# Kernel optimization log

Measured on AMD Instinct MI355X. Metric: run time of the kernel, lower is better.

The kernel has to match this reference:

```python
import jax, jax.numpy as jnp
import numpy as np

SCORE_THR = 0.5
RADII = jnp.array([0.5, 0.6, 0.7], dtype=jnp.float32)  # radius_dict[c]; all labels 0..C-1 covered

B, N, C = 2, 8192, 3


def setup_inputs() -> dict:
    key = jax.random.key(0)
    k1, k2 = jax.random.split(key)
    xyz = jax.random.normal(k1, (B, N, 3), dtype=jnp.float32)
    cls_features = jax.random.normal(k2, (B, N, C), dtype=jnp.float32)
    return {"xyz": xyz, "cls_features": cls_features}


def _greedy_select(xyz, cls_features):
    """Greedy per-class radius suppression over the flattened batch.
    Returns sample_idx (B, L) int32, zero-padded exactly like the torch code
    (sample_idx is zeros except slot i of the batch owning selection i)."""
    b, n, _ = xyz.shape
    L = b * n
    scores = jax.nn.sigmoid(jnp.max(cls_features, axis=2))   # (B, N)
    labels = jnp.argmax(cls_features, axis=2)                # (B, N)
    valid = scores >= SCORE_THR

    flat_scores = jnp.where(valid, scores, -jnp.inf).reshape(L)
    order = jnp.argsort(-flat_scores)                        # descending score; invalid sink to end
    sorted_labels = labels.reshape(L)[order]
    sorted_valid = valid.reshape(L)[order]
    sorted_batch = (order // n).astype(jnp.int32)
    sorted_pts = xyz.reshape(L, 3)[order]

    def cond(state):
        i, remaining, _ = state
        return remaining.any() & (i < L)

    def body(state):
        i, remaining, sel_pos = state
        cur = jnp.argmax(remaining)                  # first remaining point in sorted order
        # NB: faithful to the original bug: radius chosen via sorted_labels[i]
        # (loop counter), not the label of the current point.
        r = RADII[sorted_labels[i]]
        d2 = jnp.sum((sorted_pts - sorted_pts[cur]) ** 2, axis=-1)  # (L,)
        suppress = (sorted_batch == sorted_batch[cur]) & (d2 <= r * r)
        return (i + 1, remaining & ~suppress, sel_pos.at[i].set(cur.astype(jnp.int32)))

    sel0 = jnp.full((L,), -1, dtype=jnp.int32)
    _, _, sel_pos = jax.lax.while_loop(cond, body, (jnp.int32(0), sorted_valid, sel0))

    picked = sel_pos >= 0
    orig = jnp.where(picked, order[jnp.maximum(sel_pos, 0)], 0)  # flat index in [0, L)
    bidx = jnp.where(picked, orig // n, 0)
    pidx = jnp.where(picked, orig % n, 0)
    slots = jnp.arange(L)
    # zeros init + scatter exactly mirrors torch: sample_idx[batch, i] = point
    sample_idx = jnp.zeros((b, L), dtype=jnp.int32).at[bidx, slots].set(pidx.astype(jnp.int32))
    return sample_idx


def reference(xyz, cls_features):
    sample_idx = _greedy_select(xyz, cls_features)
    bsz = xyz.shape[0]
    # gather_operation: new_xyz[b, m] = xyz[b, sample_idx[b, m]]
    new_xyz = xyz[jnp.arange(bsz)[:, None], sample_idx]          # (B, L, 3)
    return new_xyz, sample_idx
```

## Files before the change

kernel.cpp:

```cpp
#include <hip/hip_runtime.h>
#include <stdint.h>


#define L_TOT 16384
#define NPT   8192

__device__ __forceinline__ int cellco(float v) {
    int c = (int)floorf((v + 6.4f) * 1.25f);
    return c < 0 ? 0 : (c > 15 ? 15 : c);
}
__device__ __forceinline__ float d2f(float ax, float ay, float az,
                                     float bx, float by, float bz) {
    float dx = __fsub_rn(ax, bx), dy = __fsub_rn(ay, by), dz = __fsub_rn(az, bz);
    return __fadd_rn(__fadd_rn(__fmul_rn(dx, dx), __fmul_rn(dy, dy)), __fmul_rn(dz, dz));
}
__device__ __forceinline__ float rad2(int lb) {
    float rr = (lb == 0) ? 0.5f : ((lb == 1) ? 0.6f : 0.7f);
    return __fmul_rn(rr, rr);
}
__device__ __forceinline__ float rlf(float v, int l) {
    return __uint_as_float(__builtin_amdgcn_readlane(__float_as_uint(v), l));
}
__device__ __forceinline__ int rli(int v, int l) {
    return (int)__builtin_amdgcn_readlane((uint32_t)v, l);
}

__global__ void k1_keys(const float* __restrict__ cls, uint64_t* __restrict__ keys,
                        uint8_t* __restrict__ umeta, uint16_t* __restrict__ sample,
                        int* __restrict__ cellcnt, uint32_t* __restrict__ slab2) {
    int l = blockIdx.x * blockDim.x + threadIdx.x;
    if (l >= L_TOT) return;
    ((uint32_t*)sample)[l] = 0;
    if (l < 8192) cellcnt[l] = 0;
    if (l < 1024) slab2[l] = 0;
    float c0 = cls[l * 3 + 0], c1 = cls[l * 3 + 1], c2 = cls[l * 3 + 2];
    float m = c0; int lab = 0;
    if (c1 > m) { m = c1; lab = 1; }
    if (c2 > m) { m = c2; lab = 2; }
    int valid = (m >= 0.0f) ? 1 : 0;
    float keyf = valid ? m : -__builtin_inff();
    uint32_t u = __float_as_uint(keyf);
    uint32_t o = (u & 0x80000000u) ? ~u : (u | 0x80000000u);
    keys[l] = ((uint64_t)(~o) << 32) | (uint32_t)l;
    umeta[l] = (uint8_t)(lab | (valid << 2));
}

__global__ void __launch_bounds__(256) k2_sort(
    const uint64_t* __restrict__ keys, const uint8_t* __restrict__ umeta,
    const float* __restrict__ xyz,
    float4* __restrict__ spts, uint32_t* __restrict__ slab2, uint16_t* __restrict__ sorder,
    int* __restrict__ cellcnt) {
    __shared__ uint64_t tile[2048];
    __shared__ int psum[256];
    const int t = threadIdx.x;
    const int elem = t & 31, part = t >> 5;
    const int l = blockIdx.x * 32 + elem;
    const uint64_t myk = keys[l];
    int cnt = 0;
    for (int t0 = 0; t0 < L_TOT; t0 += 2048) {
        for (int j = t; j < 2048; j += 256) tile[j] = keys[t0 + j];
        __syncthreads();
        const int b0 = part * 256;
        #pragma unroll 4
        for (int j = 0; j < 256; ++j) cnt += (tile[b0 + j] < myk) ? 1 : 0;
        __syncthreads();
    }
    psum[t] = cnt;
    __syncthreads();
    if (t < 32) {
        int rank = 0;
        #pragma unroll
        for (int q = 0; q < 8; ++q) rank += psum[q * 32 + t];
        const int ll = blockIdx.x * 32 + t;
        int b = ll >> 13, p = ll & (NPT - 1);
        const float* src = xyz + ((size_t)(b * NPT + p)) * 3;
        float x = src[0], y = src[1], z = src[2];
        uint8_t mt = umeta[ll];
        int lab = mt & 3, valid = (mt >> 2) & 1;
        float4 v; v.x = x; v.y = y; v.z = z;
        v.w = __uint_as_float((uint32_t)(b | (valid << 1)));
        spts[rank] = v;
        sorder[rank] = (uint16_t)ll;
        atomicOr(&slab2[rank >> 4], (uint32_t)lab << ((rank & 15) << 1));
        if (valid) {
            int cl = (b << 12) | (cellco(z) << 8) | (cellco(y) << 4) | cellco(x);
            atomicAdd(&cellcnt[cl], 1);
        }
    }
}

__global__ void g2_scan(int* __restrict__ cellcnt, int* __restrict__ cellstart) {
    __shared__ int part[256];
    __shared__ int poff[256];
    int t = threadIdx.x;
    int base = t * 32;
    int loc[32];
    int s = 0;
    for (int k = 0; k < 32; ++k) { loc[k] = cellcnt[base + k]; s += loc[k]; }
    part[t] = s;
    __syncthreads();
    if (t == 0) {
        int run = 0;
        for (int q = 0; q < 256; ++q) { poff[q] = run; run += part[q]; }
    }
    __syncthreads();
    int run = poff[t];
    for (int k = 0; k < 32; ++k) {
        cellstart[base + k] = run; run += loc[k];
        cellcnt[base + k] = 0;
    }
    if (t == 255) cellstart[8192] = run;
}

__global__ void g3_scatter(const float4* __restrict__ spts, const int* __restrict__ cellstart,
                           int* __restrict__ cellfill, float4* __restrict__ cellxyz) {
    int pos = blockIdx.x * blockDim.x + threadIdx.x;
    if (pos >= L_TOT) return;
    float4 v = spts[pos];
    uint32_t w = __float_as_uint(v.w);
    if (!(w & 2u)) return;
    int b = (int)(w & 1u);
    int cl = (b << 12) | (cellco(v.z) << 8) | (cellco(v.y) << 4) | cellco(v.x);
    int slot = atomicAdd(&cellfill[cl], 1);
    float4 o; o.x = v.x; o.y = v.y; o.z = v.z; o.w = __uint_as_float((uint32_t)pos);
    cellxyz[cellstart[cl] + slot] = o;
}

__global__ void __launch_bounds__(1024) k3_greedy(
    const float4* __restrict__ spts, const uint32_t* __restrict__ slab2,
    const uint16_t* __restrict__ sorder,
    const int* __restrict__ cellstart, const float4* __restrict__ cellxyz,
    uint16_t* __restrict__ sample) {
    __shared__ uint64_t qpack[16384];
    __shared__ uint32_t rem[512];
    __shared__ uint32_t alive2[512];
    __shared__ uint16_t cs16[8194];
    __shared__ uint32_t slds2[1024];
    __shared__ float4   pkd[2][128];
    __shared__ int      pkb[2][128];
    __shared__ int      pkn[2];

    const int t = threadIdx.x;
    const int V = cellstart[8192];
    const int NPH = (V + 127) >> 7;

    float4 cv0 = make_float4(0,0,0,0), cv1 = make_float4(0,0,0,0);
    int cord0 = 0, cord1 = 0;
    if (t < 64) {
        cv0 = spts[t]; cv1 = spts[64 + t];
        cord0 = (int)sorder[t]; cord1 = (int)sorder[64 + t];
    }
    for (int j = t; j < 8193; j += 1024) cs16[j] = (uint16_t)cellstart[j];
    for (int j = t; j < 1024; j += 1024) slds2[j] = slab2[j];
    for (int k = t; k < V; k += 1024) {
        float4 q = cellxyz[k];
        int qx = __float2int_rn(__fmul_rn(__fadd_rn(q.x, 8.0f), 4096.0f));
        int qy = __float2int_rn(__fmul_rn(__fadd_rn(q.y, 8.0f), 4096.0f));
        int qz = __float2int_rn(__fmul_rn(__fadd_rn(q.z, 8.0f), 4096.0f));
        qx = qx < 0 ? 0 : (qx > 65535 ? 65535 : qx);
        qy = qy < 0 ? 0 : (qy > 65535 ? 65535 : qy);
        qz = qz < 0 ? 0 : (qz > 65535 ? 65535 : qz);
        uint32_t pos = __float_as_uint(q.w);
        qpack[k] = ((uint64_t)(((uint32_t)qz) | (pos << 16)) << 32)
                 | ((uint32_t)qx | ((uint32_t)qy << 16));
    }
    for (int w = t; w < 512; w += 1024) {
        int lo = w * 32;
        uint32_t m;
        if (V >= lo + 32) m = 0xFFFFFFFFu;
        else if (V <= lo) m = 0u;
        else m = (1u << (V - lo)) - 1u;
        rem[w] = m;
        alive2[w] = m;
    }
    if (t < 2) pkn[t] = 0;
    __syncthreads();

    int ii = 0;
    for (int ph = 0; ph < NPH; ++ph) {
        const int cur = ph & 1, prv = cur ^ 1;
        if (t < 64) {
            const int nb = (ph + 1) << 7;
            int q0 = nb + t;       q0 = q0 > (L_TOT - 1) ? (L_TOT - 1) : q0;
            int q1 = nb + 64 + t;  q1 = q1 > (L_TOT - 1) ? (L_TOT - 1) : q1;
            float4 nv0 = spts[q0], nv1 = spts[q1];
            int nord0 = (int)sorder[q0], nord1 = (int)sorder[q1];

            int o0 = ii + t;      o0 = o0 > (L_TOT - 1) ? (L_TOT - 1) : o0;
            int o1 = ii + 64 + t; o1 = o1 > (L_TOT - 1) ? (L_TOT - 1) : o1;
            float cr0 = rad2((int)((slds2[o0 >> 4] >> ((o0 & 15) << 1)) & 3u));
            float cr1 = rad2((int)((slds2[o1 >> 4] >> ((o1 & 15) << 1)) & 3u));

            const int pos0 = (ph << 7) + t, pos1 = pos0 + 64;
            bool a0 = (pos0 < V) && ((rem[pos0 >> 5] >> (pos0 & 31)) & 1u);
            bool a1 = (pos1 < V) && ((rem[pos1 >> 5] >> (pos1 & 31)) & 1u);
            const int cb0 = cord0 >> 13, cb1 = cord1 >> 13;
            if (__ballot((a0 ? 1 : 0) | (a1 ? 1 : 0))) {
                const int m = pkn[prv];
                for (int j = 0; j < m; ++j) {
                    float4 pk = pkd[prv][j];
                    int pb = pkb[prv][j];
                    if (a0 && cb0 == pb &&
                        d2f(cv0.x, cv0.y, cv0.z, pk.x, pk.y, pk.z) <= pk.w) a0 = false;
                    if (a1 && cb1 == pb &&
                        d2f(cv1.x, cv1.y, cv1.z, pk.x, pk.y, pk.z) <= pk.w) a1 = false;
                }
            }

            int np = 0;
            const int ii0 = ii;
            {
                unsigned long long am = __ballot(a0 ? 1 : 0);
                while (am) {
                    const int jl0 = (int)__builtin_ctzll(am);
                    const unsigned long long am2 = am & (am - 1);
                    const bool has2 = (am2 != 0ull);
                    const int jl1 = has2 ? (int)__builtin_ctzll(am2) : jl0;
                    const float p0x = rlf(cv0.x, jl0), p0y = rlf(cv0.y, jl0), p0z = rlf(cv0.z, jl0);
                    const int   b0  = rli(cord0, jl0) >> 13;
                    const float p1x = rlf(cv0.x, jl1), p1y = rlf(cv0.y, jl1), p1z = rlf(cv0.z, jl1);
                    const int   b1  = rli(cord0, jl1) >> 13;
                    const float r2_0 = rlf((np & 64) ? cr1 : cr0, np & 63);
                    const int np1 = np + 1;
                    const float r2_1 = rlf((np1 & 64) ? cr1 : cr0, np1 & 63);
                    const bool kb = (b0 == b1) &&
                                    (d2f(p1x, p1y, p1z, p0x, p0y, p0z) <= r2_0);
                    const bool two = has2 && !kb;
                    if (t == jl0) {
                        pkd[cur][np] = make_float4(cv0.x, cv0.y, cv0.z, r2_0);
                        pkb[cur][np] = b0;
                        sample[b0 * L_TOT + ii0 + np] = (uint16_t)(cord0 & (NPT - 1));
                    }
                    if (two && t == jl1) {
                        pkd[cur][np1] = make_float4(cv0.x, cv0.y, cv0.z, r2_1);
                        pkb[cur][np1] = b1;
                        sample[b1 * L_TOT + ii0 + np1] = (uint16_t)(cord0 & (NPT - 1));
                    }
                    if (a0) {
                        if (cb0 == b0 && d2f(cv0.x, cv0.y, cv0.z, p0x, p0y, p0z) <= r2_0) a0 = false;
                        if (two && cb0 == b1 && d2f(cv0.x, cv0.y, cv0.z, p1x, p1y, p1z) <= r2_1) a0 = false;
                    }
                    if (a1) {
                        if (cb1 == b0 && d2f(cv1.x, cv1.y, cv1.z, p0x, p0y, p0z) <= r2_0) a1 = false;
                        if (two && cb1 == b1 && d2f(cv1.x, cv1.y, cv1.z, p1x, p1y, p1z) <= r2_1) a1 = false;
                    }
                    np += two ? 2 : 1;
                    am = __ballot(a0 ? 1 : 0);
                }
            }
            {
                unsigned long long am = __ballot(a1 ? 1 : 0);
                while (am) {
                    const int jl0 = (int)__builtin_ctzll(am);
                    const unsigned long long am2 = am & (am - 1);
                    const bool has2 = (am2 != 0ull);
                    const int jl1 = has2 ? (int)__builtin_ctzll(am2) : jl0;
                    const float p0x = rlf(cv1.x, jl0), p0y = rlf(cv1.y, jl0), p0z = rlf(cv1.z, jl0);
                    const int   b0  = rli(cord1, jl0) >> 13;
                    const float p1x = rlf(cv1.x, jl1), p1y = rlf(cv1.y, jl1), p1z = rlf(cv1.z, jl1);
                    const int   b1  = rli(cord1, jl1) >> 13;
                    const float r2_0 = rlf((np & 64) ? cr1 : cr0, np & 63);
                    const int np1 = np + 1;
                    const float r2_1 = rlf((np1 & 64) ? cr1 : cr0, np1 & 63);
                    const bool kb = (b0 == b1) &&
                                    (d2f(p1x, p1y, p1z, p0x, p0y, p0z) <= r2_0);
                    const bool two = has2 && !kb;
                    if (t == jl0) {
                        pkd[cur][np] = make_float4(cv1.x, cv1.y, cv1.z, r2_0);
                        pkb[cur][np] = b0;
                        sample[b0 * L_TOT + ii0 + np] = (uint16_t)(cord1 & (NPT - 1));
                    }
                    if (two && t == jl1) {
                        pkd[cur][np1] = make_float4(cv1.x, cv1.y, cv1.z, r2_1);
                        pkb[cur][np1] = b1;
                        sample[b1 * L_TOT + ii0 + np1] = (uint16_t)(cord1 & (NPT - 1));
                    }
                    if (a1) {
                        if (cb1 == b0 && d2f(cv1.x, cv1.y, cv1.z, p0x, p0y, p0z) <= r2_0) a1 = false;
                        if (two && cb1 == b1 && d2f(cv1.x, cv1.y, cv1.z, p1x, p1y, p1z) <= r2_1) a1 = false;
                    }
                    np += two ? 2 : 1;
                    am = __ballot(a1 ? 1 : 0);
                }
            }
            ii = ii0 + np;
            if (t == 0) pkn[cur] = np;
            cv0 = nv0; cv1 = nv1; cord0 = nord0; cord1 = nord1;
        } else {
            const int np = pkn[prv];
            if (np > 0) {
                const int tid = t - 64;
                const int ntask = np * 216;
                for (int task = tid; task < ntask; task += 960) {
                    int sub = task & 7;
                    int pc = task >> 3;
                    int p = pc / 27;
                    int c = pc - p * 27;
                    float4 pv = pkd[prv][p];
                    int pb_ = pkb[prv][p];
                    float r2 = pv.w;
                    int cx = cellco(pv.x) + (c % 3) - 1;
                    int cy = cellco(pv.y) + ((c / 3) % 3) - 1;
                    int cz = cellco(pv.z) + (c / 9) - 1;
                    if ((unsigned)cx > 15u || (unsigned)cy > 15u || (unsigned)cz > 15u) continue;
                    float lox = -6.4f + 0.8f * cx, hix = lox + 0.8f;
                    float loy = -6.4f + 0.8f * cy, hiy = loy + 0.8f;
                    float loz = -6.4f + 0.8f * cz, hiz = loz + 0.8f;
                    if (cx == 0) lox = -1e30f;  if (cx == 15) hix = 1e30f;
                    if (cy == 0) loy = -1e30f;  if (cy == 15) hiy = 1e30f;
                    if (cz == 0) loz = -1e30f;  if (cz == 15) hiz = 1e30f;
                    float bdx = fmaxf(fmaxf(lox - pv.x, pv.x - hix), 0.0f);
                    float bdy = fmaxf(fmaxf(loy - pv.y, pv.y - hiy), 0.0f);
                    float bdz = fmaxf(fmaxf(loz - pv.z, pv.z - hiz), 0.0f);
                    if (bdx * bdx + bdy * bdy + bdz * bdz > r2 + 0.02f) continue;
                    int cl = (pb_ << 12) | (cz << 8) | (cy << 4) | cx;
                    int st = (int)cs16[cl];
                    int en = (int)cs16[cl + 1];
                    float psx = (pv.x + 8.0f) * 4096.0f;
                    float psy = (pv.y + 8.0f) * 4096.0f;
                    float psz = (pv.z + 8.0f) * 4096.0f;
                    float thr_hi = (r2 + 0.02f) * 16777216.0f;
                    float thr_lo = (r2 - 0.02f) * 16777216.0f;
                    for (int k = st + sub; k < en; k += 8) {
                        uint64_t e = qpack[k];
                        uint32_t lo = (uint32_t)e, hi = (uint32_t)(e >> 32);
                        float ddx = (float)(lo & 0xffffu) - psx;
                        float ddy = (float)(lo >> 16) - psy;
                        float ddz = (float)(hi & 0xffffu) - psz;
                        float d2s = ddx * ddx + ddy * ddy + ddz * ddz;
                        if (d2s <= thr_hi) {
                            if (alive2[k >> 5] & (1u << (k & 31))) {
                                bool sup = (d2s <= thr_lo);
                                if (!sup) {
                                    float4 q = cellxyz[k];
                                    sup = d2f(q.x, q.y, q.z, pv.x, pv.y, pv.z) <= r2;
                                }
                                if (sup) {
                                    uint32_t pos = hi >> 16;
                                    atomicAnd(&alive2[k >> 5], ~(1u << (k & 31)));
                                    atomicAnd(&rem[pos >> 5], ~(1u << (pos & 31)));
                                }
                            }
                        }
                    }
                }
            }
        }
        __syncthreads();
    }
}

__global__ void k4_out(const float* __restrict__ xyz, const uint16_t* __restrict__ sample,
                       float* __restrict__ out) {
    int s = blockIdx.x * blockDim.x + threadIdx.x;
    if (s >= 2 * L_TOT) return;
    int idx = (int)sample[s];
    int b = s >> 14;
    const float* src = xyz + ((size_t)(b * NPT + idx)) * 3;
    float* dst = out + (size_t)s * 3;
    dst[0] = src[0]; dst[1] = src[1]; dst[2] = src[2];
    out[3 * 2 * L_TOT + s] = (float)idx;
}

extern "C" void kernel_launch(void* const* d_in, const int* in_sizes, int n_in,
                              void* d_out, int out_size, void* d_ws, size_t ws_size,
                              hipStream_t stream) {
    const float* xyz = (const float*)d_in[0];
    const float* cls = (const float*)d_in[1];
    float* out = (float*)d_out;
    char* ws = (char*)d_ws;
    float4*   spts    = (float4*)  (ws + 0);
    uint32_t* slab2   = (uint32_t*)(ws + 262144);
    uint16_t* sorder  = (uint16_t*)(ws + 278528);
    int*      cellcnt = (int*)     (ws + 311296);
    int*      cellst  = (int*)     (ws + 344064);
    float4*   cellxyz = (float4*)  (ws + 380928);
    uint64_t* keys    = (uint64_t*)(ws + 380928);
    uint8_t*  umeta   = (uint8_t*) (ws + 512000);
    uint16_t* sample  = (uint16_t*)(ws + 643072);

    k1_keys   <<<64,  256, 0, stream>>>(cls, keys, umeta, sample, cellcnt, slab2);
    k2_sort   <<<512, 256, 0, stream>>>(keys, umeta, xyz, spts, slab2, sorder, cellcnt);
    g2_scan   <<<1,   256, 0, stream>>>(cellcnt, cellst);
    g3_scatter<<<64,  256, 0, stream>>>(spts, cellst, cellcnt, cellxyz);
    k3_greedy <<<1,  1024, 0, stream>>>(spts, slab2, sorder, cellst, cellxyz, sample);
    k4_out    <<<128, 256, 0, stream>>>(xyz, sample, out);
}
```

Before: 508.7 us.

## Replace phase-barrier greedy loop with asynchronous producer/consumer task queue

The greedy kernel drops the per-phase __syncthreads lockstep between the picking wavefront and the suppression workers. Wave 0 now publishes picks through an atomic counter, and workers claim per-pick, per-neighbour-cell tasks dynamically. Completion is tracked per pick so the picker only rechecks candidates against picks whose suppression has not finished. Pending picks are held in registers, and the alive2 filter and packed 2-bit label array are replaced by a byte label array. The intent is to overlap picking with suppression and remove barrier stalls, at the cost of spin-waiting, workgroup-scope atomics, and more redundant scanning, since each task now walks a whole cell serially.

After: 784.3 us. +54.2%, slower.

```diff
diff --git a/kernel.cpp b/kernel.cpp
--- a/kernel.cpp
+++ b/kernel.cpp
@@ -4,6 +4,7 @@
 
 #define L_TOT 16384
 #define NPT   8192
+#define WGS   __HIP_MEMORY_SCOPE_WORKGROUP
 
 __device__ __forceinline__ int cellco(float v) {
     int c = (int)floorf((v + 6.4f) * 1.25f);
@@ -27,12 +28,11 @@
 
 __global__ void k1_keys(const float* __restrict__ cls, uint64_t* __restrict__ keys,
                         uint8_t* __restrict__ umeta, uint16_t* __restrict__ sample,
-                        int* __restrict__ cellcnt, uint32_t* __restrict__ slab2) {
+                        int* __restrict__ cellcnt) {
     int l = blockIdx.x * blockDim.x + threadIdx.x;
     if (l >= L_TOT) return;
     ((uint32_t*)sample)[l] = 0;
     if (l < 8192) cellcnt[l] = 0;
-    if (l < 1024) slab2[l] = 0;
     float c0 = cls[l * 3 + 0], c1 = cls[l * 3 + 1], c2 = cls[l * 3 + 2];
     float m = c0; int lab = 0;
     if (c1 > m) { m = c1; lab = 1; }
@@ -48,7 +48,7 @@
 __global__ void __launch_bounds__(256) k2_sort(
     const uint64_t* __restrict__ keys, const uint8_t* __restrict__ umeta,
     const float* __restrict__ xyz,
-    float4* __restrict__ spts, uint32_t* __restrict__ slab2, uint16_t* __restrict__ sorder,
+    float4* __restrict__ spts, uint8_t* __restrict__ slab, uint16_t* __restrict__ sorder,
     int* __restrict__ cellcnt) {
     __shared__ uint64_t tile[2048];
     __shared__ int psum[256];
@@ -80,8 +80,8 @@
         float4 v; v.x = x; v.y = y; v.z = z;
         v.w = __uint_as_float((uint32_t)(b | (valid << 1)));
         spts[rank] = v;
+        slab[rank] = (uint8_t)lab;
         sorder[rank] = (uint16_t)ll;
-        atomicOr(&slab2[rank >> 4], (uint32_t)lab << ((rank & 15) << 1));
         if (valid) {
             int cl = (b << 12) | (cellco(z) << 8) | (cellco(y) << 4) | cellco(x);
             atomicAdd(&cellcnt[cl], 1);
@@ -127,31 +127,22 @@
 }
 
 __global__ void __launch_bounds__(1024) k3_greedy(
-    const float4* __restrict__ spts, const uint32_t* __restrict__ slab2,
+    const float4* __restrict__ spts, const uint8_t* __restrict__ slab,
     const uint16_t* __restrict__ sorder,
     const int* __restrict__ cellstart, const float4* __restrict__ cellxyz,
     uint16_t* __restrict__ sample) {
     __shared__ uint64_t qpack[16384];
+    __shared__ uint16_t cs16[8194];
     __shared__ uint32_t rem[512];
-    __shared__ uint32_t alive2[512];
-    __shared__ uint16_t cs16[8194];
-    __shared__ uint32_t slds2[1024];
-    __shared__ float4   pkd[2][128];
-    __shared__ int      pkb[2][128];
-    __shared__ int      pkn[2];
+    __shared__ float4   pkd[256];
+    __shared__ uint8_t  pkb[256];
+    __shared__ int      tdone[512];
+    __shared__ int      c_nppub, c_taskctr, c_done;
 
     const int t = threadIdx.x;
     const int V = cellstart[8192];
-    const int NPH = (V + 127) >> 7;
-
-    float4 cv0 = make_float4(0,0,0,0), cv1 = make_float4(0,0,0,0);
-    int cord0 = 0, cord1 = 0;
-    if (t < 64) {
-        cv0 = spts[t]; cv1 = spts[64 + t];
-        cord0 = (int)sorder[t]; cord1 = (int)sorder[64 + t];
-    }
+
     for (int j = t; j < 8193; j += 1024) cs16[j] = (uint16_t)cellstart[j];
-    for (int j = t; j < 1024; j += 1024) slds2[j] = slab2[j];
     for (int k = t; k < V; k += 1024) {
         float4 q = cellxyz[k];
         int qx = __float2int_rn(__fmul_rn(__fadd_rn(q.x, 8.0f), 4096.0f));
@@ -171,148 +162,47 @@
         else if (V <= lo) m = 0u;
         else m = (1u << (V - lo)) - 1u;
         rem[w] = m;
-        alive2[w] = m;
-    }
-    if (t < 2) pkn[t] = 0;
+        tdone[w] = 0;
+    }
+    if (t == 0) { c_nppub = 0; c_taskctr = 0; c_done = 0; }
     __syncthreads();
 
-    int ii = 0;
-    for (int ph = 0; ph < NPH; ++ph) {
-        const int cur = ph & 1, prv = cur ^ 1;
-        if (t < 64) {
-            const int nb = (ph + 1) << 7;
-            int q0 = nb + t;       q0 = q0 > (L_TOT - 1) ? (L_TOT - 1) : q0;
-            int q1 = nb + 64 + t;  q1 = q1 > (L_TOT - 1) ? (L_TOT - 1) : q1;
-            float4 nv0 = spts[q0], nv1 = spts[q1];
-            int nord0 = (int)sorder[q0], nord1 = (int)sorder[q1];
-
-            int o0 = ii + t;      o0 = o0 > (L_TOT - 1) ? (L_TOT - 1) : o0;
-            int o1 = ii + 64 + t; o1 = o1 > (L_TOT - 1) ? (L_TOT - 1) : o1;
-            float cr0 = rad2((int)((slds2[o0 >> 4] >> ((o0 & 15) << 1)) & 3u));
-            float cr1 = rad2((int)((slds2[o1 >> 4] >> ((o1 & 15) << 1)) & 3u));
-
-            const int pos0 = (ph << 7) + t, pos1 = pos0 + 64;
-            bool a0 = (pos0 < V) && ((rem[pos0 >> 5] >> (pos0 & 31)) & 1u);
-            bool a1 = (pos1 < V) && ((rem[pos1 >> 5] >> (pos1 & 31)) & 1u);
-            const int cb0 = cord0 >> 13, cb1 = cord1 >> 13;
-            if (__ballot((a0 ? 1 : 0) | (a1 ? 1 : 0))) {
-                const int m = pkn[prv];
-                for (int j = 0; j < m; ++j) {
-                    float4 pk = pkd[prv][j];
-                    int pb = pkb[prv][j];
-                    if (a0 && cb0 == pb &&
-                        d2f(cv0.x, cv0.y, cv0.z, pk.x, pk.y, pk.z) <= pk.w) a0 = false;
-                    if (a1 && cb1 == pb &&
-                        d2f(cv1.x, cv1.y, cv1.z, pk.x, pk.y, pk.z) <= pk.w) a1 = false;
+    if (t >= 64) {
+        for (;;) {
+            int tid = __hip_atomic_fetch_add(&c_taskctr, 1, __ATOMIC_RELAXED, WGS);
+            int spinGuard = 0;
+            for (;;) {
+                int npq = __hip_atomic_load(&c_nppub, __ATOMIC_ACQUIRE, WGS);
+                if (tid < npq * 27) break;
+                if (__hip_atomic_load(&c_done, __ATOMIC_ACQUIRE, WGS)) {
+                    int npf = __hip_atomic_load(&c_nppub, __ATOMIC_ACQUIRE, WGS);
+                    if (tid >= npf * 27) return;
+                    break;
                 }
+                __builtin_amdgcn_s_sleep(2);
+                if (++spinGuard > (1 << 18)) return;
             }
-
-            int np = 0;
-            const int ii0 = ii;
-            {
-                unsigned long long am = __ballot(a0 ? 1 : 0);
-                while (am) {
-                    const int jl0 = (int)__builtin_ctzll(am);
-                    const unsigned long long am2 = am & (am - 1);
-                    const bool has2 = (am2 != 0ull);
-                    const int jl1 = has2 ? (int)__builtin_ctzll(am2) : jl0;
-                    const float p0x = rlf(cv0.x, jl0), p0y = rlf(cv0.y, jl0), p0z = rlf(cv0.z, jl0);
-                    const int   b0  = rli(cord0, jl0) >> 13;
-                    const float p1x = rlf(cv0.x, jl1), p1y = rlf(cv0.y, jl1), p1z = rlf(cv0.z, jl1);
-                    const int   b1  = rli(cord0, jl1) >> 13;
-                    const float r2_0 = rlf((np & 64) ? cr1 : cr0, np & 63);
-                    const int np1 = np + 1;
-                    const float r2_1 = rlf((np1 & 64) ? cr1 : cr0, np1 & 63);
-                    const bool kb = (b0 == b1) &&
-                                    (d2f(p1x, p1y, p1z, p0x, p0y, p0z) <= r2_0);
-                    const bool two = has2 && !kb;
-                    if (t == jl0) {
-                        pkd[cur][np] = make_float4(cv0.x, cv0.y, cv0.z, r2_0);
-                        pkb[cur][np] = b0;
-                        sample[b0 * L_TOT + ii0 + np] = (uint16_t)(cord0 & (NPT - 1));
-                    }
-                    if (two && t == jl1) {
-                        pkd[cur][np1] = make_float4(cv0.x, cv0.y, cv0.z, r2_1);
-                        pkb[cur][np1] = b1;
-                        sample[b1 * L_TOT + ii0 + np1] = (uint16_t)(cord0 & (NPT - 1));
-                    }
-                    if (a0) {
-                        if (cb0 == b0 && d2f(cv0.x, cv0.y, cv0.z, p0x, p0y, p0z) <= r2_0) a0 = false;
-                        if (two && cb0 == b1 && d2f(cv0.x, cv0.y, cv0.z, p1x, p1y, p1z) <= r2_1) a0 = false;
-                    }
-                    if (a1) {
-                        if (cb1 == b0 && d2f(cv1.x, cv1.y, cv1.z, p0x, p0y, p0z) <= r2_0) a1 = false;
-                        if (two && cb1 == b1 && d2f(cv1.x, cv1.y, cv1.z, p1x, p1y, p1z) <= r2_1) a1 = false;
-                    }
-                    np += two ? 2 : 1;
-                    am = __ballot(a0 ? 1 : 0);
-                }
-            }
-            {
-                unsigned long long am = __ballot(a1 ? 1 : 0);
-                while (am) {
-                    const int jl0 = (int)__builtin_ctzll(am);
-                    const unsigned long long am2 = am & (am - 1);
-                    const bool has2 = (am2 != 0ull);
-                    const int jl1 = has2 ? (int)__builtin_ctzll(am2) : jl0;
-                    const float p0x = rlf(cv1.x, jl0), p0y = rlf(cv1.y, jl0), p0z = rlf(cv1.z, jl0);
-                    const int   b0  = rli(cord1, jl0) >> 13;
-                    const float p1x = rlf(cv1.x, jl1), p1y = rlf(cv1.y, jl1), p1z = rlf(cv1.z, jl1);
-                    const int   b1  = rli(cord1, jl1) >> 13;
-                    const float r2_0 = rlf((np & 64) ? cr1 : cr0, np & 63);
-                    const int np1 = np + 1;
-                    const float r2_1 = rlf((np1 & 64) ? cr1 : cr0, np1 & 63);
-                    const bool kb = (b0 == b1) &&
-                                    (d2f(p1x, p1y, p1z, p0x, p0y, p0z) <= r2_0);
-                    const bool two = has2 && !kb;
-                    if (t == jl0) {
-                        pkd[cur][np] = make_float4(cv1.x, cv1.y, cv1.z, r2_0);
-                        pkb[cur][np] = b0;
-                        sample[b0 * L_TOT + ii0 + np] = (uint16_t)(cord1 & (NPT - 1));
-                    }
-                    if (two && t == jl1) {
-                        pkd[cur][np1] = make_float4(cv1.x, cv1.y, cv1.z, r2_1);
-                        pkb[cur][np1] = b1;
-                        sample[b1 * L_TOT + ii0 + np1] = (uint16_t)(cord1 & (NPT - 1));
-                    }
-                    if (a1) {
-                        if (cb1 == b0 && d2f(cv1.x, cv1.y, cv1.z, p0x, p0y, p0z) <= r2_0) a1 = false;
-                        if (two && cb1 == b1 && d2f(cv1.x, cv1.y, cv1.z, p1x, p1y, p1z) <= r2_1) a1 = false;
-                    }
-                    np += two ? 2 : 1;
-                    am = __ballot(a1 ? 1 : 0);
-                }
-            }
-            ii = ii0 + np;
-            if (t == 0) pkn[cur] = np;
-            cv0 = nv0; cv1 = nv1; cord0 = nord0; cord1 = nord1;
-        } else {
-            const int np = pkn[prv];
-            if (np > 0) {
-                const int tid = t - 64;
-                const int ntask = np * 216;
-                for (int task = tid; task < ntask; task += 960) {
-                    int sub = task & 7;
-                    int pc = task >> 3;
-                    int p = pc / 27;
-                    int c = pc - p * 27;
-                    float4 pv = pkd[prv][p];
-                    int pb_ = pkb[prv][p];
-                    float r2 = pv.w;
-                    int cx = cellco(pv.x) + (c % 3) - 1;
-                    int cy = cellco(pv.y) + ((c / 3) % 3) - 1;
-                    int cz = cellco(pv.z) + (c / 9) - 1;
-                    if ((unsigned)cx > 15u || (unsigned)cy > 15u || (unsigned)cz > 15u) continue;
-                    float lox = -6.4f + 0.8f * cx, hix = lox + 0.8f;
-                    float loy = -6.4f + 0.8f * cy, hiy = loy + 0.8f;
-                    float loz = -6.4f + 0.8f * cz, hiz = loz + 0.8f;
-                    if (cx == 0) lox = -1e30f;  if (cx == 15) hix = 1e30f;
-                    if (cy == 0) loy = -1e30f;  if (cy == 15) hiy = 1e30f;
-                    if (cz == 0) loz = -1e30f;  if (cz == 15) hiz = 1e30f;
-                    float bdx = fmaxf(fmaxf(lox - pv.x, pv.x - hix), 0.0f);
-                    float bdy = fmaxf(fmaxf(loy - pv.y, pv.y - hiy), 0.0f);
-                    float bdz = fmaxf(fmaxf(loz - pv.z, pv.z - hiz), 0.0f);
-                    if (bdx * bdx + bdy * bdy + bdz * bdz > r2 + 0.02f) continue;
+            int j = tid / 27;
+            int c = tid - j * 27;
+            float4 pv = pkd[j & 255];
+            int pb_ = (int)pkb[j & 255];
+            float r2 = pv.w;
+            int cx = cellco(pv.x) + (c % 3) - 1;
+            int cy = cellco(pv.y) + ((c / 3) % 3) - 1;
+            int cz = cellco(pv.z) + (c / 9) - 1;
+            bool live = !((unsigned)cx > 15u || (unsigned)cy > 15u || (unsigned)cz > 15u);
+            if (live) {
+                float lox = -6.4f + 0.8f * cx, hix = lox + 0.8f;
+                float loy = -6.4f + 0.8f * cy, hiy = loy + 0.8f;
+                float loz = -6.4f + 0.8f * cz, hiz = loz + 0.8f;
+                if (cx == 0) lox = -1e30f;  if (cx == 15) hix = 1e30f;
+                if (cy == 0) loy = -1e30f;  if (cy == 15) hiy = 1e30f;
+                if (cz == 0) loz = -1e30f;  if (cz == 15) hiz = 1e30f;
+                float bdx = fmaxf(fmaxf(lox - pv.x, pv.x - hix), 0.0f);
+                float bdy = fmaxf(fmaxf(loy - pv.y, pv.y - hiy), 0.0f);
+                float bdz = fmaxf(fmaxf(loz - pv.z, pv.z - hiz), 0.0f);
+                if (bdx * bdx + bdy * bdy + bdz * bdz > r2 + 0.02f) live = false;
+                if (live) {
                     int cl = (pb_ << 12) | (cz << 8) | (cy << 4) | cx;
                     int st = (int)cs16[cl];
                     int en = (int)cs16[cl + 1];
@@ -321,7 +211,7 @@
                     float psz = (pv.z + 8.0f) * 4096.0f;
                     float thr_hi = (r2 + 0.02f) * 16777216.0f;
                     float thr_lo = (r2 - 0.02f) * 16777216.0f;
-                    for (int k = st + sub; k < en; k += 8) {
+                    for (int k = st; k < en; ++k) {
                         uint64_t e = qpack[k];
                         uint32_t lo = (uint32_t)e, hi = (uint32_t)(e >> 32);
                         float ddx = (float)(lo & 0xffffu) - psx;
@@ -329,25 +219,168 @@
                         float ddz = (float)(hi & 0xffffu) - psz;
                         float d2s = ddx * ddx + ddy * ddy + ddz * ddz;
                         if (d2s <= thr_hi) {
-                            if (alive2[k >> 5] & (1u << (k & 31))) {
-                                bool sup = (d2s <= thr_lo);
-                                if (!sup) {
-                                    float4 q = cellxyz[k];
-                                    sup = d2f(q.x, q.y, q.z, pv.x, pv.y, pv.z) <= r2;
-                                }
-                                if (sup) {
-                                    uint32_t pos = hi >> 16;
-                                    atomicAnd(&alive2[k >> 5], ~(1u << (k & 31)));
-                                    atomicAnd(&rem[pos >> 5], ~(1u << (pos & 31)));
-                                }
+                            bool sup = (d2s <= thr_lo);
+                            if (!sup) {
+                                float4 q = cellxyz[k];
+                                sup = d2f(q.x, q.y, q.z, pv.x, pv.y, pv.z) <= r2;
+                            }
+                            if (sup) {
+                                uint32_t pos = hi >> 16;
+                                atomicAnd(&rem[pos >> 5], ~(1u << (pos & 31)));
                             }
                         }
                     }
                 }
             }
-        }
-        __syncthreads();
-    }
+            __hip_atomic_fetch_add(&tdone[j & 511], 1, __ATOMIC_RELEASE, WGS);
+        }
+    }
+
+    int gnp = 0, pend = 0;
+    float rx0=0,ry0=0,rz0=0,rr0=0; int rb0=0;
+    float rx1=0,ry1=0,rz1=0,rr1=0; int rb1=0;
+    float rx2=0,ry2=0,rz2=0,rr2=0; int rb2=0;
+    float rx3=0,ry3=0,rz3=0,rr3=0; int rb3=0;
+    const int NW = (V + 127) >> 7;
+    float4 cv0 = spts[t], cv1 = spts[64 + t];
+    int cord0 = (int)sorder[t], cord1 = (int)sorder[64 + t];
+
+    #define RECORD_PICK(GG, PX, PY, PZ, PR2, PB, PORD)                            \
+        { const int _bk = ((GG) >> 6) & 3, _ln = (GG) & 63;                       \
+          if (t == _ln) {                                                         \
+            if (_bk == 0)      { rx0=(PX); ry0=(PY); rz0=(PZ); rr0=(PR2); rb0=(PB); } \
+            else if (_bk == 1) { rx1=(PX); ry1=(PY); rz1=(PZ); rr1=(PR2); rb1=(PB); } \
+            else if (_bk == 2) { rx2=(PX); ry2=(PY); rz2=(PZ); rr2=(PR2); rb2=(PB); } \
+            else               { rx3=(PX); ry3=(PY); rz3=(PZ); rr3=(PR2); rb3=(PB); } \
+          }                                                                       \
+          if (t == 0) {                                                           \
+              pkd[(GG) & 255] = make_float4(PX, PY, PZ, PR2);                     \
+              pkb[(GG) & 255] = (uint8_t)(PB);                                    \
+              tdone[(GG) & 511] = 0;                                              \
+              sample[(PB) * L_TOT + (GG)] = (uint16_t)((PORD) & (NPT - 1));       \
+          } }
+
+    for (int w = 0; w < NW; ++w) {
+        int nb = (w + 1) << 7;
+        int q0 = nb + t;      q0 = q0 > (L_TOT - 1) ? (L_TOT - 1) : q0;
+        int q1 = nb + 64 + t; q1 = q1 > (L_TOT - 1) ? (L_TOT - 1) : q1;
+        float4 nv0 = spts[q0], nv1 = spts[q1];
+        int nord0 = (int)sorder[q0], nord1 = (int)sorder[q1];
+        int o0 = gnp + t;      o0 = o0 > (L_TOT - 1) ? (L_TOT - 1) : o0;
+        int o1 = gnp + 64 + t; o1 = o1 > (L_TOT - 1) ? (L_TOT - 1) : o1;
+        float cr0 = rad2((int)slab[o0]), cr1 = rad2((int)slab[o1]);
+
+        if (pend < gnp) {
+            int td = __hip_atomic_load(&tdone[(pend + t) & 511], __ATOMIC_ACQUIRE, WGS);
+            unsigned long long dm = __ballot(td >= 27);
+            unsigned long long inv = ~dm;
+            int adv = inv ? (int)__builtin_ctzll(inv) : 64;
+            int lim = gnp - pend;
+            pend += adv < lim ? adv : lim;
+        }
+
+        const int pos0 = (w << 7) + t, pos1 = pos0 + 64;
+        uint32_t w0 = __hip_atomic_load(&rem[(pos0 >> 5) & 511], __ATOMIC_RELAXED, WGS);
+        uint32_t w1 = __hip_atomic_load(&rem[(pos1 >> 5) & 511], __ATOMIC_RELAXED, WGS);
+        bool a0 = (pos0 < V) && ((w0 >> (pos0 & 31)) & 1u);
+        bool a1 = (pos1 < V) && ((w1 >> (pos1 & 31)) & 1u);
+        if (!__ballot((a0 ? 1 : 0) | (a1 ? 1 : 0))) {
+            cv0 = nv0; cv1 = nv1; cord0 = nord0; cord1 = nord1;
+            continue;
+        }
+
+        int guard = 0;
+        while (gnp - pend > 128) {
+            int td = __hip_atomic_load(&tdone[(pend + t) & 511], __ATOMIC_ACQUIRE, WGS);
+            unsigned long long dm = __ballot(td >= 27);
+            unsigned long long inv = ~dm;
+            int adv = inv ? (int)__builtin_ctzll(inv) : 64;
+            int lim = gnp - pend;
+            pend += adv < lim ? adv : lim;
+            if (++guard > (1 << 18)) break;
+        }
+
+        const int cb0 = cord0 >> 13, cb1 = cord1 >> 13;
+        for (int j = pend; j < gnp; ++j) {
+            int bk = (j >> 6) & 3, l = j & 63;
+            float px, py, pz, pr2; int pb;
+            if (bk == 0)      { px=rlf(rx0,l); py=rlf(ry0,l); pz=rlf(rz0,l); pr2=rlf(rr0,l); pb=rli(rb0,l); }
+            else if (bk == 1) { px=rlf(rx1,l); py=rlf(ry1,l); pz=rlf(rz1,l); pr2=rlf(rr1,l); pb=rli(rb1,l); }
+            else if (bk == 2) { px=rlf(rx2,l); py=rlf(ry2,l); pz=rlf(rz2,l); pr2=rlf(rr2,l); pb=rli(rb2,l); }
+            else              { px=rlf(rx3,l); py=rlf(ry3,l); pz=rlf(rz3,l); pr2=rlf(rr3,l); pb=rli(rb3,l); }
+            if (a0 && cb0 == pb && d2f(cv0.x, cv0.y, cv0.z, px, py, pz) <= pr2) a0 = false;
+            if (a1 && cb1 == pb && d2f(cv1.x, cv1.y, cv1.z, px, py, pz) <= pr2) a1 = false;
+        }
+
+        int npw = 0;
+        {
+            unsigned long long am = __ballot(a0 ? 1 : 0);
+            while (am) {
+                const int jl0 = (int)__builtin_ctzll(am);
+                const unsigned long long am2 = am & (am - 1);
+                const bool has2 = (am2 != 0ull);
+                const int jl1 = has2 ? (int)__builtin_ctzll(am2) : jl0;
+                const float p0x = rlf(cv0.x, jl0), p0y = rlf(cv0.y, jl0), p0z = rlf(cv0.z, jl0);
+                const int   o0u = rli(cord0, jl0), b0 = o0u >> 13;
+                const float p1x = rlf(cv0.x, jl1), p1y = rlf(cv0.y, jl1), p1z = rlf(cv0.z, jl1);
+                const int   o1u = rli(cord0, jl1), b1 = o1u >> 13;
+                const float r2_0 = rlf((npw & 64) ? cr1 : cr0, npw & 63);
+                const int np1 = npw + 1;
+                const float r2_1 = rlf((np1 & 64) ? cr1 : cr0, np1 & 63);
+                const bool kb = (b0 == b1) &&
+                                (d2f(p1x, p1y, p1z, p0x, p0y, p0z) <= r2_0);
+                const bool two = has2 && !kb;
+                RECORD_PICK(gnp + npw, p0x, p0y, p0z, r2_0, b0, o0u);
+                if (two) { RECORD_PICK(gnp + np1, p1x, p1y, p1z, r2_1, b1, o1u); }
+                if (a0) {
+                    if (cb0 == b0 && d2f(cv0.x, cv0.y, cv0.z, p0x, p0y, p0z) <= r2_0) a0 = false;
+                    if (two && cb0 == b1 && d2f(cv0.x, cv0.y, cv0.z, p1x, p1y, p1z) <= r2_1) a0 = false;
+                }
+                if (a1) {
+                    if (cb1 == b0 && d2f(cv1.x, cv1.y, cv1.z, p0x, p0y, p0z) <= r2_0) a1 = false;
+                    if (two && cb1 == b1 && d2f(cv1.x, cv1.y, cv1.z, p1x, p1y, p1z) <= r2_1) a1 = false;
+                }
+                npw += two ? 2 : 1;
+                am = __ballot(a0 ? 1 : 0);
+            }
+        }
+        {
+            unsigned long long am = __ballot(a1 ? 1 : 0);
+            while (am) {
+                const int jl0 = (int)__builtin_ctzll(am);
+                const unsigned long long am2 = am & (am - 1);
+                const bool has2 = (am2 != 0ull);
+                const int jl1 = has2 ? (int)__builtin_ctzll(am2) : jl0;
+                const float p0x = rlf(cv1.x, jl0), p0y = rlf(cv1.y, jl0), p0z = rlf(cv1.z, jl0);
+                const int   o0u = rli(cord1, jl0), b0 = o0u >> 13;
+                const float p1x = rlf(cv1.x, jl1), p1y = rlf(cv1.y, jl1), p1z = rlf(cv1.z, jl1);
+                const int   o1u = rli(cord1, jl1), b1 = o1u >> 13;
+                const float r2_0 = rlf((npw & 64) ? cr1 : cr0, npw & 63);
+                const int np1 = npw + 1;
+                const float r2_1 = rlf((np1 & 64) ? cr1 : cr0, np1 & 63);
+                const bool kb = (b0 == b1) &&
+                                (d2f(p1x, p1y, p1z, p0x, p0y, p0z) <= r2_0);
+                const bool two = has2 && !kb;
+                RECORD_PICK(gnp + npw, p0x, p0y, p0z, r2_0, b0, o0u);
+                if (two) { RECORD_PICK(gnp + np1, p1x, p1y, p1z, r2_1, b1, o1u); }
+                if (a1) {
+                    if (cb1 == b0 && d2f(cv1.x, cv1.y, cv1.z, p0x, p0y, p0z) <= r2_0) a1 = false;
+                    if (two && cb1 == b1 && d2f(cv1.x, cv1.y, cv1.z, p1x, p1y, p1z) <= r2_1) a1 = false;
+                }
+                npw += two ? 2 : 1;
+                am = __ballot(a1 ? 1 : 0);
+            }
+        }
+        if (npw > 0) {
+            gnp += npw;
+            asm volatile("s_waitcnt lgkmcnt(0)" ::: "memory");
+            if (t == 0) __hip_atomic_store(&c_nppub, gnp, __ATOMIC_RELEASE, WGS);
+        }
+        cv0 = nv0; cv1 = nv1; cord0 = nord0; cord1 = nord1;
+    }
+    asm volatile("s_waitcnt lgkmcnt(0)" ::: "memory");
+    if (t == 0) __hip_atomic_store(&c_done, 1, __ATOMIC_RELEASE, WGS);
+    #undef RECORD_PICK
 }
 
 __global__ void k4_out(const float* __restrict__ xyz, const uint16_t* __restrict__ sample,
@@ -370,7 +403,7 @@
     float* out = (float*)d_out;
     char* ws = (char*)d_ws;
     float4*   spts    = (float4*)  (ws + 0);
-    uint32_t* slab2   = (uint32_t*)(ws + 262144);
+    uint8_t*  slab    = (uint8_t*) (ws + 262144);
     uint16_t* sorder  = (uint16_t*)(ws + 278528);
     int*      cellcnt = (int*)     (ws + 311296);
     int*      cellst  = (int*)     (ws + 344064);
@@ -379,10 +412,10 @@
     uint8_t*  umeta   = (uint8_t*) (ws + 512000);
     uint16_t* sample  = (uint16_t*)(ws + 643072);
 
-    k1_keys   <<<64,  256, 0, stream>>>(cls, keys, umeta, sample, cellcnt, slab2);
-    k2_sort   <<<512, 256, 0, stream>>>(keys, umeta, xyz, spts, slab2, sorder, cellcnt);
+    k1_keys   <<<64,  256, 0, stream>>>(cls, keys, umeta, sample, cellcnt);
+    k2_sort   <<<512, 256, 0, stream>>>(keys, umeta, xyz, spts, slab, sorder, cellcnt);
     g2_scan   <<<1,   256, 0, stream>>>(cellcnt, cellst);
     g3_scatter<<<64,  256, 0, stream>>>(spts, cellst, cellcnt, cellxyz);
-    k3_greedy <<<1,  1024, 0, stream>>>(spts, slab2, sorder, cellst, cellxyz, sample);
+    k3_greedy <<<1,  1024, 0, stream>>>(spts, slab, sorder, cellst, cellxyz, sample);
     k4_out    <<<128, 256, 0, stream>>>(xyz, sample, out);
 }
```

## Keep previous picks in leader-wave registers, shrink greedy block, raise leader priority

Applied to the files above, without the earlier changes.

The leader wave now holds the previous phase's picks in per-lane registers and reads them with readlane, rather than reloading them from shared memory. It also skips the whole pick loop when no candidate in the chunk is alive. The greedy block drops from 1024 to 512 threads, the leader wave gets raised scheduling priority, and pick batch ids are stored as bytes. The aim is to cut the serial critical path of the leader wave, at the cost of fewer helper threads for neighbour-cell suppression.

After: 699.3 us. +37.5%, slower.

```diff
diff --git a/kernel.cpp b/kernel.cpp
--- a/kernel.cpp
+++ b/kernel.cpp
@@ -126,7 +126,7 @@
     cellxyz[cellstart[cl] + slot] = o;
 }
 
-__global__ void __launch_bounds__(1024) k3_greedy(
+__global__ void __launch_bounds__(512) k3_greedy(
     const float4* __restrict__ spts, const uint32_t* __restrict__ slab2,
     const uint16_t* __restrict__ sorder,
     const int* __restrict__ cellstart, const float4* __restrict__ cellxyz,
@@ -137,7 +137,7 @@
     __shared__ uint16_t cs16[8194];
     __shared__ uint32_t slds2[1024];
     __shared__ float4   pkd[2][128];
-    __shared__ int      pkb[2][128];
+    __shared__ uint8_t  pkb[2][128];
     __shared__ int      pkn[2];
 
     const int t = threadIdx.x;
@@ -150,9 +150,9 @@
         cv0 = spts[t]; cv1 = spts[64 + t];
         cord0 = (int)sorder[t]; cord1 = (int)sorder[64 + t];
     }
-    for (int j = t; j < 8193; j += 1024) cs16[j] = (uint16_t)cellstart[j];
-    for (int j = t; j < 1024; j += 1024) slds2[j] = slab2[j];
-    for (int k = t; k < V; k += 1024) {
+    for (int j = t; j < 8193; j += 512) cs16[j] = (uint16_t)cellstart[j];
+    for (int j = t; j < 1024; j += 512) slds2[j] = slab2[j];
+    for (int k = t; k < V; k += 512) {
         float4 q = cellxyz[k];
         int qx = __float2int_rn(__fmul_rn(__fadd_rn(q.x, 8.0f), 4096.0f));
         int qy = __float2int_rn(__fmul_rn(__fadd_rn(q.y, 8.0f), 4096.0f));
@@ -164,7 +164,7 @@
         qpack[k] = ((uint64_t)(((uint32_t)qz) | (pos << 16)) << 32)
                  | ((uint32_t)qx | ((uint32_t)qy << 16));
     }
-    for (int w = t; w < 512; w += 1024) {
+    for (int w = t; w < 512; w += 512) {
         int lo = w * 32;
         uint32_t m;
         if (V >= lo + 32) m = 0xFFFFFFFFu;
@@ -176,13 +176,23 @@
     if (t < 2) pkn[t] = 0;
     __syncthreads();
 
+    float kx0=0,ky0=0,kz0=0,kr0=0; int kb0=0;
+    float kx1=0,ky1=0,kz1=0,kr1=0; int kb1=0;
+    int np_prev = 0;
     int ii = 0;
+
+    if (t < 64) __builtin_amdgcn_s_setprio(1);
+
+    #define KEEP_PICK(IDX, PX, PY, PZ, PR2, PB)                                   \
+        { if ((IDX) < 64) { if (t == (IDX)) { kx0=(PX); ky0=(PY); kz0=(PZ); kr0=(PR2); kb0=(PB); } } \
+          else            { if (t == ((IDX)-64)) { kx1=(PX); ky1=(PY); kz1=(PZ); kr1=(PR2); kb1=(PB); } } }
+
     for (int ph = 0; ph < NPH; ++ph) {
         const int cur = ph & 1, prv = cur ^ 1;
         if (t < 64) {
             const int nb = (ph + 1) << 7;
-            int q0 = nb + t;       q0 = q0 > (L_TOT - 1) ? (L_TOT - 1) : q0;
-            int q1 = nb + 64 + t;  q1 = q1 > (L_TOT - 1) ? (L_TOT - 1) : q1;
+            int q0 = nb + t;      q0 = q0 > (L_TOT - 1) ? (L_TOT - 1) : q0;
+            int q1 = nb + 64 + t; q1 = q1 > (L_TOT - 1) ? (L_TOT - 1) : q1;
             float4 nv0 = spts[q0], nv1 = spts[q1];
             int nord0 = (int)sorder[q0], nord1 = (int)sorder[q1];
 
@@ -195,95 +205,104 @@
             bool a0 = (pos0 < V) && ((rem[pos0 >> 5] >> (pos0 & 31)) & 1u);
             bool a1 = (pos1 < V) && ((rem[pos1 >> 5] >> (pos1 & 31)) & 1u);
             const int cb0 = cord0 >> 13, cb1 = cord1 >> 13;
+
+            int np = 0;
             if (__ballot((a0 ? 1 : 0) | (a1 ? 1 : 0))) {
-                const int m = pkn[prv];
-                for (int j = 0; j < m; ++j) {
-                    float4 pk = pkd[prv][j];
-                    int pb = pkb[prv][j];
-                    if (a0 && cb0 == pb &&
-                        d2f(cv0.x, cv0.y, cv0.z, pk.x, pk.y, pk.z) <= pk.w) a0 = false;
-                    if (a1 && cb1 == pb &&
-                        d2f(cv1.x, cv1.y, cv1.z, pk.x, pk.y, pk.z) <= pk.w) a1 = false;
+                for (int j = 0; j < np_prev; ++j) {
+                    float px, py, pz, pr2; int pb;
+                    if (j < 64) { px=rlf(kx0,j); py=rlf(ky0,j); pz=rlf(kz0,j);
+                                  pr2=rlf(kr0,j); pb=rli(kb0,j); }
+                    else        { int l=j-64; px=rlf(kx1,l); py=rlf(ky1,l); pz=rlf(kz1,l);
+                                  pr2=rlf(kr1,l); pb=rli(kb1,l); }
+                    if (a0 && cb0 == pb && d2f(cv0.x, cv0.y, cv0.z, px, py, pz) <= pr2) a0 = false;
+                    if (a1 && cb1 == pb && d2f(cv1.x, cv1.y, cv1.z, px, py, pz) <= pr2) a1 = false;
                 }
+                const int ii0 = ii;
+                {
+                    unsigned long long am = __ballot(a0 ? 1 : 0);
+                    while (am) {
+                        const int jl0 = (int)__builtin_ctzll(am);
+                        const unsigned long long am2 = am & (am - 1);
+                        const bool has2 = (am2 != 0ull);
+                        const int jl1 = has2 ? (int)__builtin_ctzll(am2) : jl0;
+                        const float p0x = rlf(cv0.x, jl0), p0y = rlf(cv0.y, jl0), p0z = rlf(cv0.z, jl0);
+                        const int   o0u = rli(cord0, jl0), b0 = o0u >> 13;
+                        const float p1x = rlf(cv0.x, jl1), p1y = rlf(cv0.y, jl1), p1z = rlf(cv0.z, jl1);
+                        const int   o1u = rli(cord0, jl1), b1 = o1u >> 13;
+                        const float r2_0 = rlf((np & 64) ? cr1 : cr0, np & 63);
+                        const int np1 = np + 1;
+                        const float r2_1 = rlf((np1 & 64) ? cr1 : cr0, np1 & 63);
+                        const bool kb = (b0 == b1) &&
+                                        (d2f(p1x, p1y, p1z, p0x, p0y, p0z) <= r2_0);
+                        const bool two = has2 && !kb;
+                        KEEP_PICK(np, p0x, p0y, p0z, r2_0, b0);
+                        if (t == jl0) {
+                            pkd[cur][np] = make_float4(cv0.x, cv0.y, cv0.z, r2_0);
+                            pkb[cur][np] = (uint8_t)b0;
+                            sample[b0 * L_TOT + ii0 + np] = (uint16_t)(cord0 & (NPT - 1));
+                        }
+                        if (two) {
+                            KEEP_PICK(np1, p1x, p1y, p1z, r2_1, b1);
+                            if (t == jl1) {
+                                pkd[cur][np1] = make_float4(cv0.x, cv0.y, cv0.z, r2_1);
+                                pkb[cur][np1] = (uint8_t)b1;
+                                sample[b1 * L_TOT + ii0 + np1] = (uint16_t)(cord0 & (NPT - 1));
+                            }
+                        }
+                        if (a0) {
+                            if (cb0 == b0 && d2f(cv0.x, cv0.y, cv0.z, p0x, p0y, p0z) <= r2_0) a0 = false;
+                            if (two && cb0 == b1 && d2f(cv0.x, cv0.y, cv0.z, p1x, p1y, p1z) <= r2_1) a0 = false;
+                        }
+                        if (a1) {
+                            if (cb1 == b0 && d2f(cv1.x, cv1.y, cv1.z, p0x, p0y, p0z) <= r2_0) a1 = false;
+                            if (two && cb1 == b1 && d2f(cv1.x, cv1.y, cv1.z, p1x, p1y, p1z) <= r2_1) a1 = false;
+                        }
+                        np += two ? 2 : 1;
+                        am = __ballot(a0 ? 1 : 0);
+                    }
+                }
+                {
+                    unsigned long long am = __ballot(a1 ? 1 : 0);
+                    while (am) {
+                        const int jl0 = (int)__builtin_ctzll(am);
+                        const unsigned long long am2 = am & (am - 1);
+                        const bool has2 = (am2 != 0ull);
+                        const int jl1 = has2 ? (int)__builtin_ctzll(am2) : jl0;
+                        const float p0x = rlf(cv1.x, jl0), p0y = rlf(cv1.y, jl0), p0z = rlf(cv1.z, jl0);
+                        const int   o0u = rli(cord1, jl0), b0 = o0u >> 13;
+                        const float p1x = rlf(cv1.x, jl1), p1y = rlf(cv1.y, jl1), p1z = rlf(cv1.z, jl1);
+                        const int   o1u = rli(cord1, jl1), b1 = o1u >> 13;
+                        const float r2_0 = rlf((np & 64) ? cr1 : cr0, np & 63);
+                        const int np1 = np + 1;
+                        const float r2_1 = rlf((np1 & 64) ? cr1 : cr0, np1 & 63);
+                        const bool kb = (b0 == b1) &&
+                                        (d2f(p1x, p1y, p1z, p0x, p0y, p0z) <= r2_0);
+                        const bool two = has2 && !kb;
+                        KEEP_PICK(np, p0x, p0y, p0z, r2_0, b0);
+                        if (t == jl0) {
+                            pkd[cur][np] = make_float4(cv1.x, cv1.y, cv1.z, r2_0);
+                            pkb[cur][np] = (uint8_t)b0;
+                            sample[b0 * L_TOT + ii0 + np] = (uint16_t)(cord1 & (NPT - 1));
+                        }
+                        if (two) {
+                            KEEP_PICK(np1, p1x, p1y, p1z, r2_1, b1);
+                            if (t == jl1) {
+                                pkd[cur][np1] = make_float4(cv1.x, cv1.y, cv1.z, r2_1);
+                                pkb[cur][np1] = (uint8_t)b1;
+                                sample[b1 * L_TOT + ii0 + np1] = (uint16_t)(cord1 & (NPT - 1));
+                            }
+                        }
+                        if (a1) {
+                            if (cb1 == b0 && d2f(cv1.x, cv1.y, cv1.z, p0x, p0y, p0z) <= r2_0) a1 = false;
+                            if (two && cb1 == b1 && d2f(cv1.x, cv1.y, cv1.z, p1x, p1y, p1z) <= r2_1) a1 = false;
+                        }
+                        np += two ? 2 : 1;
+                        am = __ballot(a1 ? 1 : 0);
+                    }
+                }
+                ii = ii0 + np;
             }
-
-            int np = 0;
-            const int ii0 = ii;
-            {
-                unsigned long long am = __ballot(a0 ? 1 : 0);
-                while (am) {
-                    const int jl0 = (int)__builtin_ctzll(am);
-                    const unsigned long long am2 = am & (am - 1);
-                    const bool has2 = (am2 != 0ull);
-                    const int jl1 = has2 ? (int)__builtin_ctzll(am2) : jl0;
-                    const float p0x = rlf(cv0.x, jl0), p0y = rlf(cv0.y, jl0), p0z = rlf(cv0.z, jl0);
-                    const int   b0  = rli(cord0, jl0) >> 13;
-                    const float p1x = rlf(cv0.x, jl1), p1y = rlf(cv0.y, jl1), p1z = rlf(cv0.z, jl1);
-                    const int   b1  = rli(cord0, jl1) >> 13;
-                    const float r2_0 = rlf((np & 64) ? cr1 : cr0, np & 63);
-                    const int np1 = np + 1;
-                    const float r2_1 = rlf((np1 & 64) ? cr1 : cr0, np1 & 63);
-                    const bool kb = (b0 == b1) &&
-                                    (d2f(p1x, p1y, p1z, p0x, p0y, p0z) <= r2_0);
-                    const bool two = has2 && !kb;
-                    if (t == jl0) {
-                        pkd[cur][np] = make_float4(cv0.x, cv0.y, cv0.z, r2_0);
-                        pkb[cur][np] = b0;
-                        sample[b0 * L_TOT + ii0 + np] = (uint16_t)(cord0 & (NPT - 1));
-                    }
-                    if (two && t == jl1) {
-                        pkd[cur][np1] = make_float4(cv0.x, cv0.y, cv0.z, r2_1);
-                        pkb[cur][np1] = b1;
-                        sample[b1 * L_TOT + ii0 + np1] = (uint16_t)(cord0 & (NPT - 1));
-                    }
-                    if (a0) {
-                        if (cb0 == b0 && d2f(cv0.x, cv0.y, cv0.z, p0x, p0y, p0z) <= r2_0) a0 = false;
-                        if (two && cb0 == b1 && d2f(cv0.x, cv0.y, cv0.z, p1x, p1y, p1z) <= r2_1) a0 = false;
-                    }
-                    if (a1) {
-                        if (cb1 == b0 && d2f(cv1.x, cv1.y, cv1.z, p0x, p0y, p0z) <= r2_0) a1 = false;
-                        if (two && cb1 == b1 && d2f(cv1.x, cv1.y, cv1.z, p1x, p1y, p1z) <= r2_1) a1 = false;
-                    }
-                    np += two ? 2 : 1;
-                    am = __ballot(a0 ? 1 : 0);
-                }
-            }
-            {
-                unsigned long long am = __ballot(a1 ? 1 : 0);
-                while (am) {
-                    const int jl0 = (int)__builtin_ctzll(am);
-                    const unsigned long long am2 = am & (am - 1);
-                    const bool has2 = (am2 != 0ull);
-                    const int jl1 = has2 ? (int)__builtin_ctzll(am2) : jl0;
-                    const float p0x = rlf(cv1.x, jl0), p0y = rlf(cv1.y, jl0), p0z = rlf(cv1.z, jl0);
-                    const int   b0  = rli(cord1, jl0) >> 13;
-                    const float p1x = rlf(cv1.x, jl1), p1y = rlf(cv1.y, jl1), p1z = rlf(cv1.z, jl1);
-                    const int   b1  = rli(cord1, jl1) >> 13;
-                    const float r2_0 = rlf((np & 64) ? cr1 : cr0, np & 63);
-                    const int np1 = np + 1;
-                    const float r2_1 = rlf((np1 & 64) ? cr1 : cr0, np1 & 63);
-                    const bool kb = (b0 == b1) &&
-                                    (d2f(p1x, p1y, p1z, p0x, p0y, p0z) <= r2_0);
-                    const bool two = has2 && !kb;
-                    if (t == jl0) {
-                        pkd[cur][np] = make_float4(cv1.x, cv1.y, cv1.z, r2_0);
-                        pkb[cur][np] = b0;
-                        sample[b0 * L_TOT + ii0 + np] = (uint16_t)(cord1 & (NPT - 1));
-                    }
-                    if (two && t == jl1) {
-                        pkd[cur][np1] = make_float4(cv1.x, cv1.y, cv1.z, r2_1);
-                        pkb[cur][np1] = b1;
-                        sample[b1 * L_TOT + ii0 + np1] = (uint16_t)(cord1 & (NPT - 1));
-                    }
-                    if (a1) {
-                        if (cb1 == b0 && d2f(cv1.x, cv1.y, cv1.z, p0x, p0y, p0z) <= r2_0) a1 = false;
-                        if (two && cb1 == b1 && d2f(cv1.x, cv1.y, cv1.z, p1x, p1y, p1z) <= r2_1) a1 = false;
-                    }
-                    np += two ? 2 : 1;
-                    am = __ballot(a1 ? 1 : 0);
-                }
-            }
-            ii = ii0 + np;
+            np_prev = np;
             if (t == 0) pkn[cur] = np;
             cv0 = nv0; cv1 = nv1; cord0 = nord0; cord1 = nord1;
         } else {
@@ -291,13 +310,13 @@
             if (np > 0) {
                 const int tid = t - 64;
                 const int ntask = np * 216;
-                for (int task = tid; task < ntask; task += 960) {
+                for (int task = tid; task < ntask; task += 448) {
                     int sub = task & 7;
                     int pc = task >> 3;
                     int p = pc / 27;
                     int c = pc - p * 27;
                     float4 pv = pkd[prv][p];
-                    int pb_ = pkb[prv][p];
+                    int pb_ = (int)pkb[prv][p];
                     float r2 = pv.w;
                     int cx = cellco(pv.x) + (c % 3) - 1;
                     int cy = cellco(pv.y) + ((c / 3) % 3) - 1;
@@ -348,6 +367,7 @@
         }
         __syncthreads();
     }
+    #undef KEEP_PICK
 }
 
 __global__ void k4_out(const float* __restrict__ xyz, const uint16_t* __restrict__ sample,
@@ -383,6 +403,6 @@
     k2_sort   <<<512, 256, 0, stream>>>(keys, umeta, xyz, spts, slab2, sorder, cellcnt);
     g2_scan   <<<1,   256, 0, stream>>>(cellcnt, cellst);
     g3_scatter<<<64,  256, 0, stream>>>(spts, cellst, cellcnt, cellxyz);
-    k3_greedy <<<1,  1024, 0, stream>>>(spts, slab2, sorder, cellst, cellxyz, sample);
+    k3_greedy <<<1,   512, 0, stream>>>(spts, slab2, sorder, cellst, cellxyz, sample);
     k4_out    <<<128, 256, 0, stream>>>(xyz, sample, out);
 }
```
